# Kernel tuning notes

Hardware: AMD Instinct MI355X
Metric: run time of the kernel (lower is better)

Reference implementation:

```python
import jax, jax.numpy as jnp
import numpy as np

EPS = 1e-06

def _feature_map(x):
    # elu(x) + 1
    return jax.nn.elu(x) + 1.0

def setup_inputs() -> dict:
    key = jax.random.key(0)
    k1, k2, k3 = jax.random.split(key, 3)
    N, L, H, D = 4, 8192, 8, 128
    queries = jax.random.normal(k1, (N, L, H, D), dtype=jnp.float32)
    keys = jax.random.normal(k2, (N, L, H, D), dtype=jnp.float32)
    values = jax.random.normal(k3, (N, L, H, D), dtype=jnp.float32)
    threshold = jnp.array([0.1], dtype=jnp.float32)
    return {"queries": queries, "keys": keys, "values": values, "threshold": threshold}

def reference(queries, keys, values, threshold):
    Q = _feature_map(queries)            # [N,L,H,D]
    K = _feature_map(keys)               # [N,L,H,D]
    v_length = values.shape[1]
    v = values / v_length                # [N,L,H,V]
    KV = jnp.einsum('nshd,nshv->nhdv', K, v)            # [N,H,D,V]
    scores = jnp.einsum('nlhd,nhd->nlh', Q, K.sum(axis=1))  # [N,L,H]
    sparse = jnp.where(scores > threshold[0], scores, jnp.zeros_like(scores))
    Z = 1.0 / (sparse + EPS)             # [N,L,H]
    out = jnp.einsum('nlhd,nhdv,nlh->nlhv', Q, KV, Z) * v_length
    return out
```

## Files before the change

kernel.cpp:

```cpp
#include <hip/hip_runtime.h>
#include <stdint.h>


#define LSEQ 8192
#define NHD  1024
#define SP   20

typedef __attribute__((ext_vector_type(4))) float f32x4;
typedef __attribute__((ext_vector_type(8))) short bf16x8;
typedef unsigned short ushort_t;

static __device__ __forceinline__ unsigned short f2bf(float x) {
  union { float f; uint32_t u; } v; v.f = x;
  uint32_t r = v.u + 0x7FFFu + ((v.u >> 16) & 1u);
  return (unsigned short)(r >> 16);
}
static __device__ __forceinline__ uint32_t pack_bf(float a, float b) {
  return (uint32_t)f2bf(a) | ((uint32_t)f2bf(b) << 16);
}
static __device__ __forceinline__ float featmap(float x) {
  return x > 0.f ? x + 1.f : __expf(x);
}

__global__ __launch_bounds__(512) void kv_direct(const float* __restrict__ keys,
                                                 const float* __restrict__ values,
                                                 float* __restrict__ kvp,
                                                 float* __restrict__ kspart) {
  __shared__ uint32_t kls[128 * SP];
  __shared__ uint32_t vls[128 * SP];
  const int tid = threadIdx.x;
  const int chunk = blockIdx.x, CH = gridDim.x;
  const int h = blockIdx.y, n = blockIdx.z, nh = n * 8 + h;
  const int lane = tid & 63, w = tid >> 6;
  const int wr = w >> 2, wc = w & 3;
  const int lr = lane & 15, lg = lane >> 4;
  const int sPer = LSEQ / CH;
  const int steps = sPer / 32;

  const size_t gb = ((size_t)n * LSEQ + (size_t)chunk * sPer) * NHD + h * 128;
  const float* gk = keys + gb;
  const float* gv = values + gb;

  const int a = lane;
  const int wslot = (2 * w) ^ (((a >> 1) & 3) << 2);
  const int wbase0 = (2 * a) * SP + wslot;
  const int wbase1 = (2 * a + 1) * SP + wslot;

  float2 kr[4], vr[4];
#pragma unroll
  for (int j = 0; j < 4; ++j) {
    size_t off = (size_t)(4 * w + j) * NHD + 2 * a;
    kr[j] = *(const float2*)(gk + off);
    vr[j] = *(const float2*)(gv + off);
  }

  f32x4 acc[4][2] = {};
  f32x4 ak[4] = {};
  bf16x8 ones;
  { uint32_t* u = (uint32_t*)&ones; u[0] = u[1] = u[2] = u[3] = 0x3F803F80u; }

  for (int t = 0; t < steps; ++t) {
    {
      uint2 kd0, kd1, vd0, vd1;
      kd0.x = pack_bf(featmap(kr[0].x), featmap(kr[1].x));
      kd0.y = pack_bf(featmap(kr[2].x), featmap(kr[3].x));
      kd1.x = pack_bf(featmap(kr[0].y), featmap(kr[1].y));
      kd1.y = pack_bf(featmap(kr[2].y), featmap(kr[3].y));
      vd0.x = pack_bf(vr[0].x, vr[1].x);
      vd0.y = pack_bf(vr[2].x, vr[3].x);
      vd1.x = pack_bf(vr[0].y, vr[1].y);
      vd1.y = pack_bf(vr[2].y, vr[3].y);
      *(uint2*)&kls[wbase0] = kd0;
      *(uint2*)&kls[wbase1] = kd1;
      *(uint2*)&vls[wbase0] = vd0;
      *(uint2*)&vls[wbase1] = vd1;
    }
    __syncthreads();
    if (t + 1 < steps) {
#pragma unroll
      for (int j = 0; j < 4; ++j) {
        size_t off = (size_t)((t + 1) * 32 + 4 * w + j) * NHD + 2 * a;
        kr[j] = *(const float2*)(gk + off);
        vr[j] = *(const float2*)(gv + off);
      }
    }
    bf16x8 af[4], bfr[2];
#pragma unroll
    for (int fr = 0; fr < 4; ++fr) {
      int d = wr * 64 + fr * 16 + lr;
      af[fr] = *(const bf16x8*)&kls[d * SP + ((4 * lg) ^ ((((d >> 2)) & 3) << 2))];
    }
#pragma unroll
    for (int fc = 0; fc < 2; ++fc) {
      int v = wc * 32 + fc * 16 + lr;
      bfr[fc] = *(const bf16x8*)&vls[v * SP + ((4 * lg) ^ ((((v >> 2)) & 3) << 2))];
    }
#pragma unroll
    for (int fr = 0; fr < 4; ++fr)
#pragma unroll
      for (int fc = 0; fc < 2; ++fc)
        acc[fr][fc] = __builtin_amdgcn_mfma_f32_16x16x32_bf16(af[fr], bfr[fc], acc[fr][fc], 0, 0, 0);
    if (wc == 0) {
#pragma unroll
      for (int fr = 0; fr < 4; ++fr)
        ak[fr] = __builtin_amdgcn_mfma_f32_16x16x32_bf16(af[fr], ones, ak[fr], 0, 0, 0);
    }
    __syncthreads();
  }

  float* dst = kvp + ((size_t)chunk * 32 + nh) * 16384;
#pragma unroll
  for (int fr = 0; fr < 4; ++fr)
#pragma unroll
    for (int fc = 0; fc < 2; ++fc) {
      int d0 = wr * 64 + fr * 16 + lg * 4;
      int v  = wc * 32 + fc * 16 + lr;
      *(float4*)(dst + (size_t)v * 128 + d0) =
          make_float4(acc[fr][fc][0], acc[fr][fc][1], acc[fr][fc][2], acc[fr][fc][3]);
    }
  if (wc == 0 && lr == 0) {
    float* ks = kspart + ((size_t)chunk * 32 + nh) * 128;
#pragma unroll
    for (int fr = 0; fr < 4; ++fr)
      *(float4*)(ks + wr * 64 + fr * 16 + lg * 4) =
          make_float4(ak[fr][0], ak[fr][1], ak[fr][2], ak[fr][3]);
  }
}

__global__ __launch_bounds__(256) void kv_merge(const float* __restrict__ kvp,
                                                const float* __restrict__ kspart,
                                                ushort_t* __restrict__ kvb,
                                                float* __restrict__ ksumg,
                                                int CH) {
  const int nh = blockIdx.x, q = blockIdx.y, tid = threadIdx.x;
  const size_t off = (size_t)nh * 16384 + q * 4096;
#pragma unroll
  for (int i = 0; i < 4; ++i) {
    size_t idx = off + (size_t)(i * 256 + tid) * 4;
    f32x4 s = {};
    for (int c = 0; c < CH; ++c)
      s += *(const f32x4*)(kvp + (size_t)c * 524288 + idx);
    *(uint2*)(kvb + idx) = make_uint2(pack_bf(s[0], s[1]), pack_bf(s[2], s[3]));
  }
  if (q == 0 && tid < 128) {
    float s = 0.f;
    for (int c = 0; c < CH; ++c) s += kspart[((size_t)c * 32 + nh) * 128 + tid];
    ksumg[nh * 128 + tid] = s;
  }
}

__global__ __launch_bounds__(256, 4) void attn_out(const float* __restrict__ q,
                                                   const ushort_t* __restrict__ kvb,
                                                   const float* __restrict__ ksumg,
                                                   const float* __restrict__ thrp,
                                                   float* __restrict__ out) {
  __shared__ __align__(16) uint32_t As[128 * 17 * 4];
  __shared__ float zrow[128];

  const int tid = threadIdx.x;
  const int mc = blockIdx.x, nh = blockIdx.y;
  const int n = nh >> 3, h = nh & 7;
  const size_t qoff = ((size_t)(n * LSEQ + mc * 128)) * NHD + h * 128;
  const float thr = thrp[0];

  const int c4 = tid & 31;
  const float4 kk = *(const float4*)(ksumg + nh * 128 + c4 * 4);

#pragma unroll
  for (int it = 0; it < 16; ++it) {
    int rr = it * 8 + (tid >> 5);
    float4 qv = *(const float4*)(q + qoff + (size_t)rr * NHD + c4 * 4);
    float f0 = featmap(qv.x), f1 = featmap(qv.y), f2 = featmap(qv.z), f3 = featmap(qv.w);
    uint32_t* dst = &As[(rr * 17 + (c4 >> 1)) * 4 + (c4 & 1) * 2];
    dst[0] = pack_bf(f0, f1);
    dst[1] = pack_bf(f2, f3);
    float p = f0 * kk.x + f1 * kk.y + f2 * kk.z + f3 * kk.w;
    p += __shfl_xor(p, 1);  p += __shfl_xor(p, 2);  p += __shfl_xor(p, 4);
    p += __shfl_xor(p, 8);  p += __shfl_xor(p, 16);
    if (c4 == 0) {
      float sp = p > thr ? p : 0.f;
      zrow[rr] = 1.f / (sp + 1e-6f);
    }
  }
  __syncthreads();

  const int lane = tid & 63;
  const int w = tid >> 6;
  const int lr = lane & 15, lg = lane >> 4;
  const ushort_t* kvp = kvb + (size_t)nh * 16384;

  f32x4 acc0[8] = {};
  f32x4 acc1[8] = {};
#pragma unroll
  for (int ks = 0; ks < 4; ++ks) {
    const int c8 = ks * 4 + lg;
    const int dof = ks * 32 + lg * 8;
    const int r0 = w * 32 + lr;
    bf16x8 a0 = *(const bf16x8*)&As[(r0 * 17 + c8) * 4];
    bf16x8 a1 = *(const bf16x8*)&As[((r0 + 16) * 17 + c8) * 4];
#pragma unroll
    for (int ct = 0; ct < 8; ++ct) {
      bf16x8 bb = *(const bf16x8*)(kvp + (size_t)((ct * 16 + lr) * 128) + dof);
      acc0[ct] = __builtin_amdgcn_mfma_f32_16x16x32_bf16(a0, bb, acc0[ct], 0, 0, 0);
      acc1[ct] = __builtin_amdgcn_mfma_f32_16x16x32_bf16(a1, bb, acc1[ct], 0, 0, 0);
    }
  }

  float z0[4], z1[4];
#pragma unroll
  for (int j = 0; j < 4; ++j) {
    z0[j] = zrow[w * 32 + lg * 4 + j];
    z1[j] = zrow[w * 32 + 16 + lg * 4 + j];
  }
  float* op = out + qoff;
#pragma unroll
  for (int ct = 0; ct < 8; ++ct)
#pragma unroll
    for (int jj = 0; jj < 4; ++jj) {
      int row = w * 32 + lg * 4 + jj;
      op[(size_t)row * NHD + ct * 16 + lr]        = acc0[ct][jj] * z0[jj];
      op[(size_t)(row + 16) * NHD + ct * 16 + lr] = acc1[ct][jj] * z1[jj];
    }
}

extern "C" void kernel_launch(void* const* d_in, const int* in_sizes, int n_in,
                              void* d_out, int out_size, void* d_ws, size_t ws_size,
                              hipStream_t stream) {
  const float* queries   = (const float*)d_in[0];
  const float* keys      = (const float*)d_in[1];
  const float* values    = (const float*)d_in[2];
  const float* threshold = (const float*)d_in[3];
  float* out = (float*)d_out;

  int CH = 16;
  while (CH > 1 &&
         (size_t)CH * (524288 + 32 * 128) * 4 + (size_t)32 * 16384 * 2 + 32 * 128 * 4 > ws_size)
    CH >>= 1;
  float* kvp     = (float*)d_ws;
  float* kspart  = kvp + (size_t)CH * 524288;
  ushort_t* kvb  = (ushort_t*)(kspart + (size_t)CH * 32 * 128);
  float* ksumg   = (float*)(kvb + (size_t)32 * 16384);

  kv_direct<<<dim3(CH, 8, 4), 512, 0, stream>>>(keys, values, kvp, kspart);
  kv_merge<<<dim3(32, 4), 256, 0, stream>>>(kvp, kspart, kvb, ksumg, CH);
  attn_out<<<dim3(64, 32), 256, 0, stream>>>(queries, kvb, ksumg, threshold, out);
}
```

Measured before the change: 176.0 us.

## Double-buffer LDS and prefetch two steps ahead in KV accumulation kernel

The K/V staging buffers in shared memory are doubled (A/B) and two sets of register prefetches are kept in flight, so each iteration needs one barrier instead of two and global loads run two steps ahead of the MFMA work. The LDS swizzle pattern is also changed to key on different address bits, aimed at reducing bank conflicts. Launch bounds now request 4 waves per SIMD minimum. The cost is twice the LDS footprint and more live registers. The loop also assumes an even number of steps.

```diff
diff --git a/kernel.cpp b/kernel.cpp
--- a/kernel.cpp
+++ b/kernel.cpp
@@ -22,12 +22,14 @@
   return x > 0.f ? x + 1.f : __expf(x);
 }
 
-__global__ __launch_bounds__(512) void kv_direct(const float* __restrict__ keys,
-                                                 const float* __restrict__ values,
-                                                 float* __restrict__ kvp,
-                                                 float* __restrict__ kspart) {
-  __shared__ uint32_t kls[128 * SP];
-  __shared__ uint32_t vls[128 * SP];
+__global__ __launch_bounds__(512, 4) void kv_direct(const float* __restrict__ keys,
+                                                    const float* __restrict__ values,
+                                                    float* __restrict__ kvp,
+                                                    float* __restrict__ kspart) {
+  __shared__ uint32_t klsA[128 * SP];
+  __shared__ uint32_t vlsA[128 * SP];
+  __shared__ uint32_t klsB[128 * SP];
+  __shared__ uint32_t vlsB[128 * SP];
   const int tid = threadIdx.x;
   const int chunk = blockIdx.x, CH = gridDim.x;
   const int h = blockIdx.y, n = blockIdx.z, nh = n * 8 + h;
@@ -42,71 +44,80 @@
   const float* gv = values + gb;
 
   const int a = lane;
-  const int wslot = (2 * w) ^ (((a >> 1) & 3) << 2);
+  const int fsw = 4 * ((a >> 2) & 3);
+  const int wslot = (2 * w) ^ fsw;
   const int wbase0 = (2 * a) * SP + wslot;
   const int wbase1 = (2 * a + 1) * SP + wslot;
-
-  float2 kr[4], vr[4];
-#pragma unroll
-  for (int j = 0; j < 4; ++j) {
-    size_t off = (size_t)(4 * w + j) * NHD + 2 * a;
-    kr[j] = *(const float2*)(gk + off);
-    vr[j] = *(const float2*)(gv + off);
-  }
 
   f32x4 acc[4][2] = {};
   f32x4 ak[4] = {};
   bf16x8 ones;
   { uint32_t* u = (uint32_t*)&ones; u[0] = u[1] = u[2] = u[3] = 0x3F803F80u; }
 
-  for (int t = 0; t < steps; ++t) {
-    {
-      uint2 kd0, kd1, vd0, vd1;
-      kd0.x = pack_bf(featmap(kr[0].x), featmap(kr[1].x));
-      kd0.y = pack_bf(featmap(kr[2].x), featmap(kr[3].x));
-      kd1.x = pack_bf(featmap(kr[0].y), featmap(kr[1].y));
-      kd1.y = pack_bf(featmap(kr[2].y), featmap(kr[3].y));
-      vd0.x = pack_bf(vr[0].x, vr[1].x);
-      vd0.y = pack_bf(vr[2].x, vr[3].x);
-      vd1.x = pack_bf(vr[0].y, vr[1].y);
-      vd1.y = pack_bf(vr[2].y, vr[3].y);
-      *(uint2*)&kls[wbase0] = kd0;
-      *(uint2*)&kls[wbase1] = kd1;
-      *(uint2*)&vls[wbase0] = vd0;
-      *(uint2*)&vls[wbase1] = vd1;
-    }
+#define ISSUE(KR, VR, T)                                        \
+  do {                                                          \
+    _Pragma("unroll") for (int j = 0; j < 4; ++j) {             \
+      size_t off = (size_t)((T) * 32 + 4 * w + j) * NHD + 2 * a;\
+      KR[j] = *(const float2*)(gk + off);                       \
+      VR[j] = *(const float2*)(gv + off);                       \
+    }                                                           \
+  } while (0)
+
+#define STAGE(KLS, VLS, KR, VR)                                 \
+  do {                                                          \
+    uint2 kd0, kd1, vd0, vd1;                                   \
+    kd0.x = pack_bf(featmap(KR[0].x), featmap(KR[1].x));        \
+    kd0.y = pack_bf(featmap(KR[2].x), featmap(KR[3].x));        \
+    kd1.x = pack_bf(featmap(KR[0].y), featmap(KR[1].y));        \
+    kd1.y = pack_bf(featmap(KR[2].y), featmap(KR[3].y));        \
+    vd0.x = pack_bf(VR[0].x, VR[1].x);                          \
+    vd0.y = pack_bf(VR[2].x, VR[3].x);                          \
+    vd1.x = pack_bf(VR[0].y, VR[1].y);                          \
+    vd1.y = pack_bf(VR[2].y, VR[3].y);                          \
+    *(uint2*)&KLS[wbase0] = kd0;                                \
+    *(uint2*)&KLS[wbase1] = kd1;                                \
+    *(uint2*)&VLS[wbase0] = vd0;                                \
+    *(uint2*)&VLS[wbase1] = vd1;                                \
+  } while (0)
+
+#define FRAGS_MFMA(KLS, VLS)                                                       \
+  do {                                                                             \
+    bf16x8 af[4], bfr[2];                                                          \
+    _Pragma("unroll") for (int fr = 0; fr < 4; ++fr) {                             \
+      int d = wr * 64 + fr * 16 + lr;                                              \
+      af[fr] = *(const bf16x8*)&KLS[d * SP + ((4 * lg) ^ (4 * ((d >> 3) & 3)))];   \
+    }                                                                              \
+    _Pragma("unroll") for (int fc = 0; fc < 2; ++fc) {                             \
+      int v = wc * 32 + fc * 16 + lr;                                              \
+      bfr[fc] = *(const bf16x8*)&VLS[v * SP + ((4 * lg) ^ (4 * ((v >> 3) & 3)))];  \
+    }                                                                              \
+    _Pragma("unroll") for (int fr = 0; fr < 4; ++fr)                               \
+      _Pragma("unroll") for (int fc = 0; fc < 2; ++fc)                             \
+        acc[fr][fc] =                                                              \
+            __builtin_amdgcn_mfma_f32_16x16x32_bf16(af[fr], bfr[fc], acc[fr][fc], 0, 0, 0); \
+    if (wc == 0) {                                                                 \
+      _Pragma("unroll") for (int fr = 0; fr < 4; ++fr)                             \
+        ak[fr] = __builtin_amdgcn_mfma_f32_16x16x32_bf16(af[fr], ones, ak[fr], 0, 0, 0); \
+    }                                                                              \
+  } while (0)
+
+  float2 krP[4], vrP[4], krQ[4], vrQ[4];
+  ISSUE(krP, vrP, 0);
+  ISSUE(krQ, vrQ, 1);
+
+  for (int t = 0; t < steps; t += 2) {
+    STAGE(klsA, vlsA, krP, vrP);
     __syncthreads();
-    if (t + 1 < steps) {
-#pragma unroll
-      for (int j = 0; j < 4; ++j) {
-        size_t off = (size_t)((t + 1) * 32 + 4 * w + j) * NHD + 2 * a;
-        kr[j] = *(const float2*)(gk + off);
-        vr[j] = *(const float2*)(gv + off);
-      }
-    }
-    bf16x8 af[4], bfr[2];
-#pragma unroll
-    for (int fr = 0; fr < 4; ++fr) {
-      int d = wr * 64 + fr * 16 + lr;
-      af[fr] = *(const bf16x8*)&kls[d * SP + ((4 * lg) ^ ((((d >> 2)) & 3) << 2))];
-    }
-#pragma unroll
-    for (int fc = 0; fc < 2; ++fc) {
-      int v = wc * 32 + fc * 16 + lr;
-      bfr[fc] = *(const bf16x8*)&vls[v * SP + ((4 * lg) ^ ((((v >> 2)) & 3) << 2))];
-    }
-#pragma unroll
-    for (int fr = 0; fr < 4; ++fr)
-#pragma unroll
-      for (int fc = 0; fc < 2; ++fc)
-        acc[fr][fc] = __builtin_amdgcn_mfma_f32_16x16x32_bf16(af[fr], bfr[fc], acc[fr][fc], 0, 0, 0);
-    if (wc == 0) {
-#pragma unroll
-      for (int fr = 0; fr < 4; ++fr)
-        ak[fr] = __builtin_amdgcn_mfma_f32_16x16x32_bf16(af[fr], ones, ak[fr], 0, 0, 0);
-    }
+    if (t + 2 < steps) ISSUE(krP, vrP, t + 2);
+    FRAGS_MFMA(klsA, vlsA);
+    STAGE(klsB, vlsB, krQ, vrQ);
     __syncthreads();
-  }
+    if (t + 3 < steps) ISSUE(krQ, vrQ, t + 3);
+    FRAGS_MFMA(klsB, vlsB);
+  }
+#undef ISSUE
+#undef STAGE
+#undef FRAGS_MFMA
 
   float* dst = kvp + ((size_t)chunk * 32 + nh) * 16384;
 #pragma unroll
```

Result: faster. 172.5 us (-2.0%).

## Split KV accumulation across value halves with smaller blocks and lighter barriers

Applied to the files above, without the earlier changes.

Replaces the 512-thread KV kernel with a 256-thread kernel where each block computes only half of the value dimension, doubling the grid so more blocks are resident per CU. Each wave now loads 8 key rows and half-width value rows per step, with a new LDS swizzle. __syncthreads is replaced by an inline waitcnt-lgkm plus s_barrier so pending global prefetches are not drained at the barrier. The cost is that the key feature map and its bf16 conversion are now done twice, once per value half, and key reads from global memory double.

```diff
diff --git a/kernel.cpp b/kernel.cpp
--- a/kernel.cpp
+++ b/kernel.cpp
@@ -22,91 +22,97 @@
   return x > 0.f ? x + 1.f : __expf(x);
 }
 
-__global__ __launch_bounds__(512) void kv_direct(const float* __restrict__ keys,
-                                                 const float* __restrict__ values,
-                                                 float* __restrict__ kvp,
-                                                 float* __restrict__ kspart) {
+#define BAR_LGKM() asm volatile("s_waitcnt lgkmcnt(0)\n\ts_barrier" ::: "memory")
+
+__global__ __launch_bounds__(256, 4) void kv_vh(const float* __restrict__ keys,
+                                                const float* __restrict__ values,
+                                                float* __restrict__ kvp,
+                                                float* __restrict__ kspart) {
   __shared__ uint32_t kls[128 * SP];
-  __shared__ uint32_t vls[128 * SP];
+  __shared__ uint32_t vls[64 * SP];
   const int tid = threadIdx.x;
   const int chunk = blockIdx.x, CH = gridDim.x;
-  const int h = blockIdx.y, n = blockIdx.z, nh = n * 8 + h;
+  const int h = blockIdx.y;
+  const int n = blockIdx.z >> 1, vh = blockIdx.z & 1;
+  const int nh = n * 8 + h;
   const int lane = tid & 63, w = tid >> 6;
-  const int wr = w >> 2, wc = w & 3;
+  const int wr = w >> 1, wc = w & 1;
   const int lr = lane & 15, lg = lane >> 4;
   const int sPer = LSEQ / CH;
   const int steps = sPer / 32;
 
   const size_t gb = ((size_t)n * LSEQ + (size_t)chunk * sPer) * NHD + h * 128;
   const float* gk = keys + gb;
-  const float* gv = values + gb;
+  const float* gv = values + gb + vh * 64;
 
   const int a = lane;
-  const int wslot = (2 * w) ^ (((a >> 1) & 3) << 2);
-  const int wbase0 = (2 * a) * SP + wslot;
-  const int wbase1 = (2 * a + 1) * SP + wslot;
-
-  float2 kr[4], vr[4];
-#pragma unroll
-  for (int j = 0; j < 4; ++j) {
-    size_t off = (size_t)(4 * w + j) * NHD + 2 * a;
-    kr[j] = *(const float2*)(gk + off);
-    vr[j] = *(const float2*)(gv + off);
-  }
+  const int fswA = 4 * ((a >> 2) & 3);
+  const int kslot = (4 * w) ^ fswA;
+  const int vloc = 2 * (a & 31);
+  const int shalf = a >> 5;
+  const int fswV = 4 * ((vloc >> 3) & 3);
+  const int vslot = (4 * w + 2 * shalf) ^ fswV;
 
   f32x4 acc[4][2] = {};
   f32x4 ak[4] = {};
   bf16x8 ones;
   { uint32_t* u = (uint32_t*)&ones; u[0] = u[1] = u[2] = u[3] = 0x3F803F80u; }
 
+#define ISSUE(T)                                                  \
+  do {                                                            \
+    _Pragma("unroll") for (int j = 0; j < 8; ++j)                 \
+      kr[j] = *(const float2*)(gk + (size_t)((T) * 32 + 8 * w + j) * NHD + 2 * a); \
+    _Pragma("unroll") for (int j = 0; j < 4; ++j)                 \
+      vr[j] = *(const float2*)(gv + (size_t)((T) * 32 + 8 * w + 4 * shalf + j) * NHD + vloc); \
+  } while (0)
+
+  float2 kr[8], vr[4];
+  ISSUE(0);
+
   for (int t = 0; t < steps; ++t) {
     {
-      uint2 kd0, kd1, vd0, vd1;
-      kd0.x = pack_bf(featmap(kr[0].x), featmap(kr[1].x));
-      kd0.y = pack_bf(featmap(kr[2].x), featmap(kr[3].x));
-      kd1.x = pack_bf(featmap(kr[0].y), featmap(kr[1].y));
-      kd1.y = pack_bf(featmap(kr[2].y), featmap(kr[3].y));
-      vd0.x = pack_bf(vr[0].x, vr[1].x);
-      vd0.y = pack_bf(vr[2].x, vr[3].x);
-      vd1.x = pack_bf(vr[0].y, vr[1].y);
-      vd1.y = pack_bf(vr[2].y, vr[3].y);
-      *(uint2*)&kls[wbase0] = kd0;
-      *(uint2*)&kls[wbase1] = kd1;
-      *(uint2*)&vls[wbase0] = vd0;
-      *(uint2*)&vls[wbase1] = vd1;
-    }
-    __syncthreads();
-    if (t + 1 < steps) {
-#pragma unroll
-      for (int j = 0; j < 4; ++j) {
-        size_t off = (size_t)((t + 1) * 32 + 4 * w + j) * NHD + 2 * a;
-        kr[j] = *(const float2*)(gk + off);
-        vr[j] = *(const float2*)(gv + off);
-      }
-    }
-    bf16x8 af[4], bfr[2];
-#pragma unroll
-    for (int fr = 0; fr < 4; ++fr) {
-      int d = wr * 64 + fr * 16 + lr;
-      af[fr] = *(const bf16x8*)&kls[d * SP + ((4 * lg) ^ ((((d >> 2)) & 3) << 2))];
-    }
-#pragma unroll
-    for (int fc = 0; fc < 2; ++fc) {
-      int v = wc * 32 + fc * 16 + lr;
-      bfr[fc] = *(const bf16x8*)&vls[v * SP + ((4 * lg) ^ ((((v >> 2)) & 3) << 2))];
-    }
-#pragma unroll
-    for (int fr = 0; fr < 4; ++fr)
-#pragma unroll
-      for (int fc = 0; fc < 2; ++fc)
-        acc[fr][fc] = __builtin_amdgcn_mfma_f32_16x16x32_bf16(af[fr], bfr[fc], acc[fr][fc], 0, 0, 0);
-    if (wc == 0) {
+      uint32_t k0[4], k1[4];
+#pragma unroll
+      for (int u = 0; u < 4; ++u) {
+        k0[u] = pack_bf(featmap(kr[2 * u].x), featmap(kr[2 * u + 1].x));
+        k1[u] = pack_bf(featmap(kr[2 * u].y), featmap(kr[2 * u + 1].y));
+      }
+      *(uint4*)&kls[(2 * a) * SP + kslot]     = make_uint4(k0[0], k0[1], k0[2], k0[3]);
+      *(uint4*)&kls[(2 * a + 1) * SP + kslot] = make_uint4(k1[0], k1[1], k1[2], k1[3]);
+      uint2 v0, v1;
+      v0.x = pack_bf(vr[0].x, vr[1].x); v0.y = pack_bf(vr[2].x, vr[3].x);
+      v1.x = pack_bf(vr[0].y, vr[1].y); v1.y = pack_bf(vr[2].y, vr[3].y);
+      *(uint2*)&vls[vloc * SP + vslot]       = v0;
+      *(uint2*)&vls[(vloc + 1) * SP + vslot] = v1;
+    }
+    BAR_LGKM();
+    if (t + 1 < steps) ISSUE(t + 1);
+    {
+      bf16x8 af[4], bfr[2];
+#pragma unroll
+      for (int fr = 0; fr < 4; ++fr) {
+        int d = wr * 64 + fr * 16 + lr;
+        af[fr] = *(const bf16x8*)&kls[d * SP + ((4 * lg) ^ (4 * ((d >> 3) & 3)))];
+      }
+#pragma unroll
+      for (int fc = 0; fc < 2; ++fc) {
+        int v = wc * 32 + fc * 16 + lr;
+        bfr[fc] = *(const bf16x8*)&vls[v * SP + ((4 * lg) ^ (4 * ((v >> 3) & 3)))];
+      }
 #pragma unroll
       for (int fr = 0; fr < 4; ++fr)
-        ak[fr] = __builtin_amdgcn_mfma_f32_16x16x32_bf16(af[fr], ones, ak[fr], 0, 0, 0);
-    }
-    __syncthreads();
-  }
+#pragma unroll
+        for (int fc = 0; fc < 2; ++fc)
+          acc[fr][fc] = __builtin_amdgcn_mfma_f32_16x16x32_bf16(af[fr], bfr[fc], acc[fr][fc], 0, 0, 0);
+      if (wc == 0 && vh == 0) {
+#pragma unroll
+        for (int fr = 0; fr < 4; ++fr)
+          ak[fr] = __builtin_amdgcn_mfma_f32_16x16x32_bf16(af[fr], ones, ak[fr], 0, 0, 0);
+      }
+    }
+    BAR_LGKM();
+  }
+#undef ISSUE
 
   float* dst = kvp + ((size_t)chunk * 32 + nh) * 16384;
 #pragma unroll
@@ -114,11 +120,11 @@
 #pragma unroll
     for (int fc = 0; fc < 2; ++fc) {
       int d0 = wr * 64 + fr * 16 + lg * 4;
-      int v  = wc * 32 + fc * 16 + lr;
+      int v  = vh * 64 + wc * 32 + fc * 16 + lr;
       *(float4*)(dst + (size_t)v * 128 + d0) =
           make_float4(acc[fr][fc][0], acc[fr][fc][1], acc[fr][fc][2], acc[fr][fc][3]);
     }
-  if (wc == 0 && lr == 0) {
+  if (wc == 0 && vh == 0 && lr == 0) {
     float* ks = kspart + ((size_t)chunk * 32 + nh) * 128;
 #pragma unroll
     for (int fr = 0; fr < 4; ++fr)
@@ -241,7 +247,7 @@
   ushort_t* kvb  = (ushort_t*)(kspart + (size_t)CH * 32 * 128);
   float* ksumg   = (float*)(kvb + (size_t)32 * 16384);
 
-  kv_direct<<<dim3(CH, 8, 4), 512, 0, stream>>>(keys, values, kvp, kspart);
+  kv_vh<<<dim3(CH, 8, 8), 256, 0, stream>>>(keys, values, kvp, kspart);
   kv_merge<<<dim3(32, 4), 256, 0, stream>>>(kvp, kspart, kvb, ksumg, CH);
   attn_out<<<dim3(64, 32), 256, 0, stream>>>(queries, kvb, ksumg, threshold, out);
 }
```

Result: no change. 177.9 us (+1.1%).

## Store bf16 KV partials, double split count, and use lighter LDS barriers

Applied to the files above, without the earlier changes.

The kv_direct kernel now writes its per-chunk KV partials as bf16 instead of fp32, so the partial-buffer traffic is halved and kv_merge reads half as many bytes. The chunk count rises from 16 to 32 to put more blocks in flight, and launch bounds ask for four blocks per CU. __syncthreads is replaced by an inline-asm lgkmcnt wait plus s_barrier, and the LDS swizzle pattern is changed. The trade-off is an extra bf16 rounding of the partial sums before accumulation, which adds precision loss. The merge also has twice as many partials to sum.

```diff
diff --git a/kernel.cpp b/kernel.cpp
--- a/kernel.cpp
+++ b/kernel.cpp
@@ -22,10 +22,12 @@
   return x > 0.f ? x + 1.f : __expf(x);
 }
 
-__global__ __launch_bounds__(512) void kv_direct(const float* __restrict__ keys,
-                                                 const float* __restrict__ values,
-                                                 float* __restrict__ kvp,
-                                                 float* __restrict__ kspart) {
+#define BAR_LGKM() asm volatile("s_waitcnt lgkmcnt(0)\n\ts_barrier" ::: "memory")
+
+__global__ __launch_bounds__(512, 4) void kv_direct(const float* __restrict__ keys,
+                                                    const float* __restrict__ values,
+                                                    ushort_t* __restrict__ kvpb,
+                                                    float* __restrict__ kspart) {
   __shared__ uint32_t kls[128 * SP];
   __shared__ uint32_t vls[128 * SP];
   const int tid = threadIdx.x;
@@ -42,22 +44,27 @@
   const float* gv = values + gb;
 
   const int a = lane;
-  const int wslot = (2 * w) ^ (((a >> 1) & 3) << 2);
+  const int fsw = 4 * ((a >> 2) & 3);
+  const int wslot = (2 * w) ^ fsw;
   const int wbase0 = (2 * a) * SP + wslot;
   const int wbase1 = (2 * a + 1) * SP + wslot;
-
-  float2 kr[4], vr[4];
-#pragma unroll
-  for (int j = 0; j < 4; ++j) {
-    size_t off = (size_t)(4 * w + j) * NHD + 2 * a;
-    kr[j] = *(const float2*)(gk + off);
-    vr[j] = *(const float2*)(gv + off);
-  }
 
   f32x4 acc[4][2] = {};
   f32x4 ak[4] = {};
   bf16x8 ones;
   { uint32_t* u = (uint32_t*)&ones; u[0] = u[1] = u[2] = u[3] = 0x3F803F80u; }
+
+#define ISSUE(T)                                                \
+  do {                                                          \
+    _Pragma("unroll") for (int j = 0; j < 4; ++j) {             \
+      size_t off = (size_t)((T) * 32 + 4 * w + j) * NHD + 2 * a;\
+      kr[j] = *(const float2*)(gk + off);                       \
+      vr[j] = *(const float2*)(gv + off);                       \
+    }                                                           \
+  } while (0)
+
+  float2 kr[4], vr[4];
+  ISSUE(0);
 
   for (int t = 0; t < steps; ++t) {
     {
@@ -75,48 +82,45 @@
       *(uint2*)&vls[wbase0] = vd0;
       *(uint2*)&vls[wbase1] = vd1;
     }
-    __syncthreads();
-    if (t + 1 < steps) {
-#pragma unroll
-      for (int j = 0; j < 4; ++j) {
-        size_t off = (size_t)((t + 1) * 32 + 4 * w + j) * NHD + 2 * a;
-        kr[j] = *(const float2*)(gk + off);
-        vr[j] = *(const float2*)(gv + off);
+    BAR_LGKM();
+    if (t + 1 < steps) ISSUE(t + 1);
+    {
+      bf16x8 af[4], bfr[2];
+#pragma unroll
+      for (int fr = 0; fr < 4; ++fr) {
+        int d = wr * 64 + fr * 16 + lr;
+        af[fr] = *(const bf16x8*)&kls[d * SP + ((4 * lg) ^ (4 * ((d >> 3) & 3)))];
       }
-    }
-    bf16x8 af[4], bfr[2];
-#pragma unroll
-    for (int fr = 0; fr < 4; ++fr) {
-      int d = wr * 64 + fr * 16 + lr;
-      af[fr] = *(const bf16x8*)&kls[d * SP + ((4 * lg) ^ ((((d >> 2)) & 3) << 2))];
-    }
-#pragma unroll
-    for (int fc = 0; fc < 2; ++fc) {
-      int v = wc * 32 + fc * 16 + lr;
-      bfr[fc] = *(const bf16x8*)&vls[v * SP + ((4 * lg) ^ ((((v >> 2)) & 3) << 2))];
-    }
-#pragma unroll
-    for (int fr = 0; fr < 4; ++fr)
-#pragma unroll
-      for (int fc = 0; fc < 2; ++fc)
-        acc[fr][fc] = __builtin_amdgcn_mfma_f32_16x16x32_bf16(af[fr], bfr[fc], acc[fr][fc], 0, 0, 0);
-    if (wc == 0) {
+#pragma unroll
+      for (int fc = 0; fc < 2; ++fc) {
+        int v = wc * 32 + fc * 16 + lr;
+        bfr[fc] = *(const bf16x8*)&vls[v * SP + ((4 * lg) ^ (4 * ((v >> 3) & 3)))];
+      }
 #pragma unroll
       for (int fr = 0; fr < 4; ++fr)
-        ak[fr] = __builtin_amdgcn_mfma_f32_16x16x32_bf16(af[fr], ones, ak[fr], 0, 0, 0);
-    }
-    __syncthreads();
-  }
-
-  float* dst = kvp + ((size_t)chunk * 32 + nh) * 16384;
+#pragma unroll
+        for (int fc = 0; fc < 2; ++fc)
+          acc[fr][fc] = __builtin_amdgcn_mfma_f32_16x16x32_bf16(af[fr], bfr[fc], acc[fr][fc], 0, 0, 0);
+      if (wc == 0) {
+#pragma unroll
+        for (int fr = 0; fr < 4; ++fr)
+          ak[fr] = __builtin_amdgcn_mfma_f32_16x16x32_bf16(af[fr], ones, ak[fr], 0, 0, 0);
+      }
+    }
+    BAR_LGKM();
+  }
+#undef ISSUE
+
+  ushort_t* dst = kvpb + ((size_t)chunk * 32 + nh) * 16384;
 #pragma unroll
   for (int fr = 0; fr < 4; ++fr)
 #pragma unroll
     for (int fc = 0; fc < 2; ++fc) {
       int d0 = wr * 64 + fr * 16 + lg * 4;
       int v  = wc * 32 + fc * 16 + lr;
-      *(float4*)(dst + (size_t)v * 128 + d0) =
-          make_float4(acc[fr][fc][0], acc[fr][fc][1], acc[fr][fc][2], acc[fr][fc][3]);
+      *(uint2*)(dst + (size_t)v * 128 + d0) =
+          make_uint2(pack_bf(acc[fr][fc][0], acc[fr][fc][1]),
+                     pack_bf(acc[fr][fc][2], acc[fr][fc][3]));
     }
   if (wc == 0 && lr == 0) {
     float* ks = kspart + ((size_t)chunk * 32 + nh) * 128;
@@ -127,7 +131,7 @@
   }
 }
 
-__global__ __launch_bounds__(256) void kv_merge(const float* __restrict__ kvp,
+__global__ __launch_bounds__(256) void kv_merge(const ushort_t* __restrict__ kvpb,
                                                 const float* __restrict__ kspart,
                                                 ushort_t* __restrict__ kvb,
                                                 float* __restrict__ ksumg,
@@ -138,8 +142,13 @@
   for (int i = 0; i < 4; ++i) {
     size_t idx = off + (size_t)(i * 256 + tid) * 4;
     f32x4 s = {};
-    for (int c = 0; c < CH; ++c)
-      s += *(const f32x4*)(kvp + (size_t)c * 524288 + idx);
+    for (int c = 0; c < CH; ++c) {
+      uint2 u = *(const uint2*)(kvpb + (size_t)c * 524288 + idx);
+      s[0] += __uint_as_float(u.x << 16);
+      s[1] += __uint_as_float(u.x & 0xFFFF0000u);
+      s[2] += __uint_as_float(u.y << 16);
+      s[3] += __uint_as_float(u.y & 0xFFFF0000u);
+    }
     *(uint2*)(kvb + idx) = make_uint2(pack_bf(s[0], s[1]), pack_bf(s[2], s[3]));
   }
   if (q == 0 && tid < 128) {
@@ -232,16 +241,16 @@
   const float* threshold = (const float*)d_in[3];
   float* out = (float*)d_out;
 
-  int CH = 16;
+  int CH = 32;
   while (CH > 1 &&
-         (size_t)CH * (524288 + 32 * 128) * 4 + (size_t)32 * 16384 * 2 + 32 * 128 * 4 > ws_size)
+         (size_t)CH * (524288 * 2 + 32 * 128 * 4) + (size_t)32 * 16384 * 2 + 32 * 128 * 4 > ws_size)
     CH >>= 1;
-  float* kvp     = (float*)d_ws;
-  float* kspart  = kvp + (size_t)CH * 524288;
+  ushort_t* kvpb = (ushort_t*)d_ws;
+  float* kspart  = (float*)(kvpb + (size_t)CH * 524288);
   ushort_t* kvb  = (ushort_t*)(kspart + (size_t)CH * 32 * 128);
   float* ksumg   = (float*)(kvb + (size_t)32 * 16384);
 
-  kv_direct<<<dim3(CH, 8, 4), 512, 0, stream>>>(keys, values, kvp, kspart);
-  kv_merge<<<dim3(32, 4), 256, 0, stream>>>(kvp, kspart, kvb, ksumg, CH);
+  kv_direct<<<dim3(CH, 8, 4), 512, 0, stream>>>(keys, values, kvpb, kspart);
+  kv_merge<<<dim3(32, 4), 256, 0, stream>>>(kvpb, kspart, kvb, ksumg, CH);
   attn_out<<<dim3(64, 32), 256, 0, stream>>>(queries, kvb, ksumg, threshold, out);
 }
```

Result: slower. 200.3 us (+13.8%).
